# Performance work log

Hardware: AMD Instinct MI355X
Metric: run time of the kernel (lower is better)

The kernel has to match this reference:

```python
import jax, jax.numpy as jnp
import numpy as np

BLOCK = 32  # 2**basic_block

def _hadamard(n):
    H = np.array([[1.0]], dtype=np.float32)
    while H.shape[0] < n:
        H = np.block([[H, H], [H, -H]])
    return H


def setup_inputs() -> dict:
    key = jax.random.key(0)
    ks = jax.random.split(key, 9)
    B, T, I, Hd, O = 64, 512, 128, 1024, 128
    sgn = lambda k, shp: jnp.where(jax.random.normal(k, shp) >= 0, 1.0, -1.0).astype(jnp.float32)
    return {
        "x": jax.random.normal(ks[0], (B, T, I), dtype=jnp.float32),
        "W_in": jax.random.normal(ks[1], (I, Hd), dtype=jnp.float32) / np.sqrt(I),
        "s1": sgn(ks[2], (Hd,)),                      # Binadamard sign vector (layer 1)
        "b1": 0.01 * jax.random.normal(ks[3], (Hd,), dtype=jnp.float32),
        "s2": sgn(ks[4], (Hd,)),                      # Binadamard sign vector (layer 2, full)
        "b2": 0.01 * jax.random.normal(ks[5], (Hd,), dtype=jnp.float32),
        "Wbn": sgn(ks[6], (Hd, Hd)) / np.sqrt(Hd),    # BinaryNorm: sign(W)/sqrt(n), materialized
        "W_out": jax.random.normal(ks[7], (Hd, O), dtype=jnp.float32) / np.sqrt(Hd),
        "b_out": jax.random.normal(ks[8], (O,), dtype=jnp.float32),
    }


def reference(x, W_in, s1, b1, s2, b2, Wbn, W_out, b_out):
    B, T, _ = x.shape
    Hd = s1.shape[0]
    Hb = jnp.asarray(_hadamard(BLOCK) / np.sqrt(BLOCK), dtype=x.dtype)   # [32,32]
    Hf = jnp.asarray(_hadamard(Hd) / np.sqrt(Hd), dtype=x.dtype)         # [Hd,Hd]
    u = jnp.einsum('bti,ih->tbh', x, W_in)  # precompute input projections, time-major

    def step(carry, u_t):
        h1, h2 = carry
        # layer 1: block-diagonal sign*Hadamard recurrence + input
        h1 = s1 * (h1.reshape(B, -1, BLOCK) @ Hb).reshape(B, Hd) + b1 + u_t
        h1b = jax.nn.relu(h1)
        # layer 2: full sign*Hadamard recurrence + binary-norm projection of h1b
        h2 = s2 * (h2 @ Hf) + b2 + h1b @ Wbn
        return (h1, h2), None

    h0 = jnp.zeros((B, Hd), dtype=x.dtype)
    (_, h2), _ = jax.lax.scan(step, (h0, h0), u)
    h2b = jax.nn.relu(h2)
    return h2b @ W_out + b_out
```

## Files before the change

### kernel.cpp

```cpp
#include <hip/hip_runtime.h>

#define B_ 64
#define T_ 512
#define I_ 128
#define H_ 1024
#define O_ 128

typedef unsigned short u16;
typedef unsigned int u32;
typedef __attribute__((ext_vector_type(8))) short short8v;
typedef __attribute__((ext_vector_type(4))) float float4v;

typedef __attribute__((address_space(1))) const void gvoid_t;
typedef __attribute__((address_space(3))) void svoid_t;

__device__ __forceinline__ u16 f2bf(float f) {
  union { float f; u32 u; } v; v.f = f;
  u32 r = v.u + 0x7FFF + ((v.u >> 16) & 1);
  return (u16)(r >> 16);
}
__device__ __forceinline__ float bf2f(u16 b) {
  union { u32 u; float f; } v; v.u = ((u32)b) << 16;
  return v.f;
}
__device__ __forceinline__ float bits2f(u32 b) {
  union { u32 u; float f; } v; v.u = b;
  return v.f;
}

__device__ __forceinline__ float fwht32(float x, int lane) {
#pragma unroll
  for (int s = 1; s <= 16; s <<= 1) {
    const float y = __shfl_xor(x, s);
    x = (lane & s) ? (y - x) : (x + y);
  }
  return x;
}

__device__ __forceinline__ void fwht32_reg(float* x) {
#pragma unroll
  for (int s = 1; s < 32; s <<= 1)
#pragma unroll
    for (int i = 0; i < 32; ++i)
      if (!(i & s)) { const float a = x[i], b = x[i | s]; x[i] = a + b; x[i | s] = a - b; }
}

__device__ __forceinline__ void transpose32(float* x, float (*T)[33], int t) {
#pragma unroll
  for (int c = 0; c < 32; ++c) T[t][c] = x[c];
#pragma unroll
  for (int c = 0; c < 32; ++c) x[c] = T[c][t];
}

__global__ __launch_bounds__(256) void prep_all(const float* __restrict__ x, const float* __restrict__ Wbn,
                                                const float* __restrict__ W_in, u16* __restrict__ xT,
                                                u16* __restrict__ WbnT, u16* __restrict__ WinT) {
  __shared__ float tl[32][33];
  const int blk = blockIdx.x;
  const int tid = threadIdx.x;
  if (blk < 1024) {
    const int bx = blk & 31, by = blk >> 5;
    const int c = tid & 31, r8 = tid >> 5;
#pragma unroll
    for (int i = 0; i < 4; ++i) {
      const int r = r8 + i * 8;
      tl[r][c] = Wbn[(size_t)(by * 32 + r) * 1024 + bx * 32 + c];
    }
    __syncthreads();
#pragma unroll
    for (int i = 0; i < 4; ++i) {
      const int r = r8 + i * 8;
      WbnT[(size_t)(bx * 32 + r) * 1024 + by * 32 + c] = f2bf(tl[c][r]);
    }
  } else if (blk < 1152) {
    const int t2 = blk - 1024;
    const int bx = t2 & 31, by = t2 >> 5;
    const int c = tid & 31, r8 = tid >> 5;
#pragma unroll
    for (int i = 0; i < 4; ++i) {
      const int r = r8 + i * 8;
      tl[r][c] = W_in[(size_t)(by * 32 + r) * 1024 + bx * 32 + c];
    }
    __syncthreads();
#pragma unroll
    for (int i = 0; i < 4; ++i) {
      const int r = r8 + i * 8;
      WinT[(size_t)(bx * 32 + r) * 128 + by * 32 + c] = f2bf(tl[c][r]);
    }
  } else {
    const int idx = (blk - 1152) * 256 + tid;
    const int i = idx & (I_ - 1);
    const int r = idx >> 7;
    const int b = r & (B_ - 1);
    const int t = r >> 6;
    xT[idx] = f2bf(x[((size_t)b * T_ + t) * I_ + i]);
  }
}

template <int K, bool BIAS>
__global__ __launch_bounds__(512) void gemm_bf16(const u16* __restrict__ A, const u16* __restrict__ Bt,
                                                 u16* __restrict__ C, const float* __restrict__ bias) {
  __shared__ u16 As[128 * 64];
  __shared__ u16 Bs[256 * 64];
  const int tid = threadIdx.x;
  const int bm = blockIdx.x, bn = blockIdx.y;
  const int lane = tid & 63, w = tid >> 6;
  const int wr = w >> 2, wc = w & 3;
  const int l16 = lane & 15, lq = lane >> 4;

  float4v acc[4][4];
#pragma unroll
  for (int mi = 0; mi < 4; ++mi)
#pragma unroll
    for (int ni = 0; ni < 4; ++ni)
#pragma unroll
      for (int j = 0; j < 4; ++j) acc[mi][ni][j] = 0.f;

  const int lrow = lane >> 3;
  const int scol = (((lane & 7) ^ lrow) << 3);
  const u16* Ag = A + (size_t)(bm * 128 + w * 16 + lrow) * K + scol;
  const u16* Bg = Bt + (size_t)(bn * 256 + w * 32 + lrow) * K + scol;

  for (int k0 = 0; k0 < K; k0 += 64) {
    __syncthreads();
#pragma unroll
    for (int i = 0; i < 2; ++i)
      __builtin_amdgcn_global_load_lds((gvoid_t*)(Ag + k0 + (size_t)i * 8 * K),
                                       (svoid_t*)&As[(w * 16 + i * 8) * 64], 16, 0, 0);
#pragma unroll
    for (int i = 0; i < 4; ++i)
      __builtin_amdgcn_global_load_lds((gvoid_t*)(Bg + k0 + (size_t)i * 8 * K),
                                       (svoid_t*)&Bs[(w * 32 + i * 8) * 64], 16, 0, 0);
    __syncthreads();
#pragma unroll
    for (int ks = 0; ks < 2; ++ks) {
      short8v a[4], bf[4];
#pragma unroll
      for (int mi = 0; mi < 4; ++mi) {
        const int row = wr * 64 + mi * 16 + l16;
        a[mi] = *(const short8v*)&As[row * 64 + (((ks * 4 + lq) ^ (row & 7)) << 3)];
      }
#pragma unroll
      for (int ni = 0; ni < 4; ++ni) {
        const int row = wc * 64 + ni * 16 + l16;
        bf[ni] = *(const short8v*)&Bs[row * 64 + (((ks * 4 + lq) ^ (row & 7)) << 3)];
      }
#pragma unroll
      for (int mi = 0; mi < 4; ++mi)
#pragma unroll
        for (int ni = 0; ni < 4; ++ni)
          acc[mi][ni] = __builtin_amdgcn_mfma_f32_16x16x32_bf16(a[mi], bf[ni], acc[mi][ni], 0, 0, 0);
    }
  }

#pragma unroll
  for (int mi = 0; mi < 4; ++mi)
#pragma unroll
    for (int ni = 0; ni < 4; ++ni) {
      const int row = bm * 128 + wr * 64 + mi * 16 + lq * 4;
      const int col = bn * 256 + wc * 64 + ni * 16 + l16;
      const float bv = BIAS ? bias[col] : 0.f;
#pragma unroll
      for (int j = 0; j < 4; ++j) C[(size_t)(row + j) * H_ + col] = f2bf(acc[mi][ni][j] + bv);
    }
}

__global__ __launch_bounds__(1024) void h1_Pinit(const float* __restrict__ s1, float* __restrict__ P) {
  const int hb = blockIdx.x;
  const int tid = threadIdx.x;
  const int j = tid >> 5, r = tid & 31;
  const int lane = tid & 63;
  const float sc = s1[hb * 32 + r] * 0.17677669529663687f;
  float x = (r == j) ? 1.f : 0.f;
  for (int it = 0; it < 16; ++it) x = sc * fwht32(x, lane);
  P[(size_t)hb * 1024 + r * 32 + j] = x;
}

__global__ __launch_bounds__(64) void h1_local(const u16* __restrict__ u, const float* __restrict__ s1,
                                               float* __restrict__ Ybuf) {
  const int g = blockIdx.x * 64 + threadIdx.x;
  const int hb = g & 31, b = (g >> 5) & 63, chunk = g >> 11;
  float x[32], sc[32];
#pragma unroll
  for (int i = 0; i < 32; i += 4) {
    const float4 s4 = *(const float4*)&s1[hb * 32 + i];
    sc[i] = s4.x * 0.17677669529663687f;
    sc[i + 1] = s4.y * 0.17677669529663687f;
    sc[i + 2] = s4.z * 0.17677669529663687f;
    sc[i + 3] = s4.w * 0.17677669529663687f;
  }
#pragma unroll
  for (int i = 0; i < 32; ++i) x[i] = 0.f;
  const u16* up = u + ((size_t)(chunk * 16) * B_ + b) * H_ + hb * 32;
#pragma unroll 2
  for (int k = 0; k < 16; ++k) {
    u32 wv[16];
#pragma unroll
    for (int j = 0; j < 4; ++j) {
      const uint4 t4 = *(const uint4*)(up + (size_t)k * (B_ * H_) + j * 8);
      wv[4 * j] = t4.x; wv[4 * j + 1] = t4.y; wv[4 * j + 2] = t4.z; wv[4 * j + 3] = t4.w;
    }
    fwht32_reg(x);
#pragma unroll
    for (int i2 = 0; i2 < 16; ++i2) {
      x[2 * i2]     = fmaf(sc[2 * i2],     x[2 * i2],     bits2f(wv[i2] << 16));
      x[2 * i2 + 1] = fmaf(sc[2 * i2 + 1], x[2 * i2 + 1], bits2f(wv[i2] & 0xFFFF0000u));
    }
  }
  float* yp = Ybuf + (size_t)g * 32;
#pragma unroll
  for (int i = 0; i < 32; i += 4) {
    float4 o; o.x = x[i]; o.y = x[i + 1]; o.z = x[i + 2]; o.w = x[i + 3];
    *(float4*)(yp + i) = o;
  }
}

__global__ __launch_bounds__(64) void h1_carry(const float* __restrict__ P, const float* __restrict__ Ybuf,
                                               float* __restrict__ Zbuf) {
  const int hpair = blockIdx.x, b = blockIdx.y;
  const int lane = threadIdx.x;
  const int r = lane & 31, hb = hpair * 2 + (lane >> 5);
  const float* Prow = P + (size_t)hb * 1024 + r * 32;
  float pr[32];
#pragma unroll
  for (int j = 0; j < 32; ++j) pr[j] = Prow[j];
  float z = 0.f;
  const int base = lane & 32;
  for (int c = 0; c < 32; ++c) {
    Zbuf[(((size_t)c * 64 + b) * 32 + hb) * 32 + r] = z;
    if (c < 31) {
      const float yv = Ybuf[(((size_t)c * 64 + b) * 32 + hb) * 32 + r];
      float zn = 0.f;
#pragma unroll
      for (int j = 0; j < 32; ++j) zn = fmaf(pr[j], __shfl(z, base + j), zn);
      z = zn + yv;
    }
  }
}

__global__ __launch_bounds__(64) void h1_apply(u16* __restrict__ u, const float* __restrict__ s1,
                                               const float* __restrict__ Zbuf) {
  const int g = blockIdx.x * 64 + threadIdx.x;
  const int hb = g & 31, b = (g >> 5) & 63, chunk = g >> 11;
  float x[32], sc[32];
#pragma unroll
  for (int i = 0; i < 32; i += 4) {
    const float4 s4 = *(const float4*)&s1[hb * 32 + i];
    sc[i] = s4.x * 0.17677669529663687f;
    sc[i + 1] = s4.y * 0.17677669529663687f;
    sc[i + 2] = s4.z * 0.17677669529663687f;
    sc[i + 3] = s4.w * 0.17677669529663687f;
  }
  const float* zp = Zbuf + (size_t)g * 32;
#pragma unroll
  for (int i = 0; i < 32; i += 4) {
    const float4 z4 = *(const float4*)(zp + i);
    x[i] = z4.x; x[i + 1] = z4.y; x[i + 2] = z4.z; x[i + 3] = z4.w;
  }
  u16* up = u + ((size_t)(chunk * 16) * B_ + b) * H_ + hb * 32;
#pragma unroll 2
  for (int k = 0; k < 16; ++k) {
    u32 wv[16];
#pragma unroll
    for (int j = 0; j < 4; ++j) {
      const uint4 t4 = *(const uint4*)(up + (size_t)k * (B_ * H_) + j * 8);
      wv[4 * j] = t4.x; wv[4 * j + 1] = t4.y; wv[4 * j + 2] = t4.z; wv[4 * j + 3] = t4.w;
    }
    fwht32_reg(x);
#pragma unroll
    for (int i2 = 0; i2 < 16; ++i2) {
      x[2 * i2]     = fmaf(sc[2 * i2],     x[2 * i2],     bits2f(wv[i2] << 16));
      x[2 * i2 + 1] = fmaf(sc[2 * i2 + 1], x[2 * i2 + 1], bits2f(wv[i2] & 0xFFFF0000u));
    }
    u32 ov[16];
#pragma unroll
    for (int i2 = 0; i2 < 16; ++i2) {
      const u32 lo = f2bf(fmaxf(x[2 * i2], 0.f));
      const u32 hi = f2bf(fmaxf(x[2 * i2 + 1], 0.f));
      ov[i2] = lo | (hi << 16);
    }
#pragma unroll
    for (int j = 0; j < 4; ++j) {
      uint4 t4; t4.x = ov[4 * j]; t4.y = ov[4 * j + 1]; t4.z = ov[4 * j + 2]; t4.w = ov[4 * j + 3];
      *(uint4*)(up + (size_t)k * (B_ * H_) + j * 8) = t4;
    }
  }
}

__global__ __launch_bounds__(256) void fwht_chunk(const u16* __restrict__ V, const float* __restrict__ s2,
                                                  u16* __restrict__ A32, u16* __restrict__ Y) {
  __shared__ float tr[4][2][32][33];
  const int wv = threadIdx.x >> 6;
  const int lane = threadIdx.x & 63;
  const int slot = lane >> 5, t = lane & 31;
  float (*T)[33] = tr[wv][slot];
  const int gs = blockIdx.x * 8 + wv * 2 + slot;

  float x[32], s0[32], s1[32];
#pragma unroll
  for (int c = 0; c < 32; ++c) {
    s0[c] = s2[t * 32 + c] * 0.03125f;
    s1[c] = s2[c * 32 + t] * 0.03125f;
  }

  if (gs < 1024) {
    const int W = gs;
#pragma unroll
    for (int c = 0; c < 32; ++c) x[c] = (t * 32 + c == W) ? 1.f : 0.f;
    for (int j = 0; j < 32; ++j) {
      if (j & 1) {
#pragma unroll
        for (int c = 0; c < 32; ++c) x[c] *= s1[c];
      } else {
#pragma unroll
        for (int c = 0; c < 32; ++c) x[c] *= s0[c];
      }
      fwht32_reg(x);
      transpose32(x, T, t);
      fwht32_reg(x);
    }
    u16* dst = A32 + (size_t)W * H_ + t * 32;
    u32 ov[16];
#pragma unroll
    for (int c = 0; c < 16; ++c) ov[c] = (u32)f2bf(x[2 * c]) | ((u32)f2bf(x[2 * c + 1]) << 16);
#pragma unroll
    for (int j = 0; j < 4; ++j) {
      uint4 t4; t4.x = ov[4 * j]; t4.y = ov[4 * j + 1]; t4.z = ov[4 * j + 2]; t4.w = ov[4 * j + 3];
      *(uint4*)(dst + j * 8) = t4;
    }
  } else {
    const int s = gs - 1024;
    const int c0 = s >> 6, b = s & 63;
    const u16* Vbase = V + ((size_t)(c0 * 32) * B_ + b) * H_;
#pragma unroll
    for (int c = 0; c < 32; ++c) x[c] = 0.f;
    for (int j = 0; j < 32; ++j) {
      const u16* vrow = Vbase + (size_t)j * (B_ * H_);
      const int pe = (j + 1) & 1;
      u32 vpk[16];
      u16 vsc[32];
      if (pe == 0) {
#pragma unroll
        for (int q = 0; q < 4; ++q) {
          const uint4 t4 = *(const uint4*)(vrow + t * 32 + q * 8);
          vpk[4 * q] = t4.x; vpk[4 * q + 1] = t4.y; vpk[4 * q + 2] = t4.z; vpk[4 * q + 3] = t4.w;
        }
      } else {
#pragma unroll
        for (int c = 0; c < 32; ++c) vsc[c] = vrow[c * 32 + t];
      }
      fwht32_reg(x);
      transpose32(x, T, t);
      fwht32_reg(x);
      if (pe == 0) {
#pragma unroll
        for (int c = 0; c < 16; ++c) {
          x[2 * c]     = fmaf(s0[2 * c],     x[2 * c],     bits2f(vpk[c] << 16));
          x[2 * c + 1] = fmaf(s0[2 * c + 1], x[2 * c + 1], bits2f(vpk[c] & 0xFFFF0000u));
        }
      } else {
#pragma unroll
        for (int c = 0; c < 32; ++c) x[c] = fmaf(s1[c], x[c], bf2f(vsc[c]));
      }
    }
    u16* dst = Y + ((size_t)c0 * B_ + b) * H_ + t * 32;
    u32 ov[16];
#pragma unroll
    for (int c = 0; c < 16; ++c) ov[c] = (u32)f2bf(x[2 * c]) | ((u32)f2bf(x[2 * c + 1]) << 16);
#pragma unroll
    for (int j = 0; j < 4; ++j) {
      uint4 t4; t4.x = ov[4 * j]; t4.y = ov[4 * j + 1]; t4.z = ov[4 * j + 2]; t4.w = ov[4 * j + 3];
      *(uint4*)(dst + j * 8) = t4;
    }
  }
}

template <bool FIRST, bool LAST>
__global__ __launch_bounds__(256) void combine(const u16* __restrict__ Zold, const u16* __restrict__ Yc,
                                               const u16* __restrict__ A32, u16* __restrict__ Znew,
                                               float* __restrict__ h2out) {
  const int rt = blockIdx.x >> 6, nt = blockIdx.x & 63;
  const int tid = threadIdx.x;
  __shared__ float red[4][16][16];
  if (!FIRST) {
    const int w = tid >> 6, lane = tid & 63, l16 = lane & 15, lq = lane >> 4;
    float4v acc = {0.f, 0.f, 0.f, 0.f};
    const u16* Ap = Zold + (size_t)(rt * 16 + l16) * H_ + w * 256 + lq * 8;
    const u16* Bp = A32 + (size_t)(nt * 16 + l16) * H_ + w * 256 + lq * 8;
#pragma unroll
    for (int ks = 0; ks < 8; ++ks) {
      short8v a = *(const short8v*)(Ap + ks * 32);
      short8v bb = *(const short8v*)(Bp + ks * 32);
      acc = __builtin_amdgcn_mfma_f32_16x16x32_bf16(a, bb, acc, 0, 0, 0);
    }
#pragma unroll
    for (int j = 0; j < 4; ++j) red[w][lq * 4 + j][l16] = acc[j];
    __syncthreads();
  } else {
    __syncthreads();
  }
  const int row = tid >> 4, col = tid & 15;
  float s = 0.f;
  if (!FIRST) s = red[0][row][col] + red[1][row][col] + red[2][row][col] + red[3][row][col];
  const int b = rt * 16 + row, n = nt * 16 + col;
  s += bf2f(Yc[(size_t)b * H_ + n]);
  if (LAST) h2out[(size_t)b * H_ + n] = s;
  else Znew[(size_t)b * H_ + n] = f2bf(s);
}

__global__ __launch_bounds__(128) void final_out(const float* __restrict__ h2, const float* __restrict__ W_out,
                                                 const float* __restrict__ b_out, float* __restrict__ out) {
  __shared__ float hrow[H_];
  const int b = blockIdx.x, o = threadIdx.x;
  for (int i = o; i < H_; i += 128) hrow[i] = fmaxf(h2[(size_t)b * H_ + i], 0.f);
  __syncthreads();
  float acc = b_out[o];
  for (int h = 0; h < H_; ++h) acc = fmaf(hrow[h], W_out[(size_t)h * O_ + o], acc);
  out[b * O_ + o] = acc;
}

extern "C" void kernel_launch(void* const* d_in, const int* in_sizes, int n_in,
                              void* d_out, int out_size, void* d_ws, size_t ws_size,
                              hipStream_t stream) {
  const float* x     = (const float*)d_in[0];
  const float* W_in  = (const float*)d_in[1];
  const float* s1    = (const float*)d_in[2];
  const float* b1    = (const float*)d_in[3];
  const float* s2    = (const float*)d_in[4];
  const float* b2    = (const float*)d_in[5];
  const float* Wbn   = (const float*)d_in[6];
  const float* W_out = (const float*)d_in[7];
  const float* b_out = (const float*)d_in[8];
  float* out = (float*)d_out;

  char* ws = (char*)d_ws;
  u16* u      = (u16*)ws;
  u16* V      = (u16*)(ws + 67108864);
  float* P1   = (float*)(ws + 67108864);
  float* Zbuf = (float*)(ws + 69206016);
  u16* xT     = (u16*)(ws + 134217728);
  float* Ybuf = (float*)(ws + 134217728);
  u16* WbnT   = (u16*)(ws + 142606336);
  u16* WinT   = (u16*)(ws + 144703488);
  u16* A32    = (u16*)(ws + 134217728);
  u16* Y      = (u16*)(ws + 136314880);
  u16* Zb0    = (u16*)(ws + 138412032);
  u16* Zb1    = (u16*)(ws + 138543104);
  float* h2   = (float*)(ws + 138674176);

  prep_all<<<17536, 256, 0, stream>>>(x, Wbn, W_in, xT, WbnT, WinT);
  h1_Pinit<<<32, 1024, 0, stream>>>(s1, P1);
  gemm_bf16<128, true><<<dim3(256, 4), 512, 0, stream>>>(xT, WinT, u, b1);
  h1_local<<<1024, 64, 0, stream>>>(u, s1, Ybuf);
  h1_carry<<<dim3(16, 64), 64, 0, stream>>>(P1, Ybuf, Zbuf);
  h1_apply<<<1024, 64, 0, stream>>>(u, s1, Zbuf);
  gemm_bf16<1024, true><<<dim3(256, 4), 512, 0, stream>>>(u, WbnT, V, b2);
  fwht_chunk<<<256, 256, 0, stream>>>(V, s2, A32, Y);

  u16* Zb[2] = {Zb0, Zb1};
  combine<true, false><<<256, 256, 0, stream>>>(nullptr, Y, A32, Zb[0], nullptr);
  for (int c = 1; c < 15; ++c)
    combine<false, false><<<256, 256, 0, stream>>>(Zb[(c + 1) & 1], Y + (size_t)c * B_ * H_, A32,
                                                   Zb[c & 1], nullptr);
  combine<false, true><<<256, 256, 0, stream>>>(Zb[0], Y + (size_t)15 * B_ * H_, A32, nullptr, h2);

  final_out<<<64, 128, 0, stream>>>(h2, W_out, b_out, out);
}
```

Measured before the change: 309.5 us.

## Replace sequential chunk combine chain with log-depth tree using squared transition matrices

The 16 sequential combine launches become a binary-tree reduction. Each level pairs chunk states and multiplies by a doubled-power transition matrix (A32, A64, A128, A256), which is computed by repeated squaring with explicit transposes. This cuts the serial dependency chain from 16 launches to about 7, but adds three full 1024x1024 bf16 matrix squarings and extra rounding from squaring in bf16, which may hurt accuracy.

```diff
diff --git a/kernel.cpp b/kernel.cpp
--- a/kernel.cpp
+++ b/kernel.cpp
@@ -375,37 +375,93 @@
   }
 }
 
-template <bool FIRST, bool LAST>
-__global__ __launch_bounds__(256) void combine(const u16* __restrict__ Zold, const u16* __restrict__ Yc,
-                                               const u16* __restrict__ A32, u16* __restrict__ Znew,
-                                               float* __restrict__ h2out) {
+template <bool LAST>
+__device__ __forceinline__ void tree_tile(const u16* X, const u16* add, const u16* P,
+                                          u16* out, float* h2out, int rt, int nt, int tid,
+                                          float (*red)[16][16]) {
+  const int w = tid >> 6, lane = tid & 63, l16 = lane & 15, lq = lane >> 4;
+  float4v acc = {0.f, 0.f, 0.f, 0.f};
+  const u16* Ap = X + (size_t)(rt * 16 + l16) * H_ + w * 256 + lq * 8;
+  const u16* Bp = P + (size_t)(nt * 16 + l16) * H_ + w * 256 + lq * 8;
+#pragma unroll
+  for (int ks = 0; ks < 8; ++ks) {
+    short8v a = *(const short8v*)(Ap + ks * 32);
+    short8v bb = *(const short8v*)(Bp + ks * 32);
+    acc = __builtin_amdgcn_mfma_f32_16x16x32_bf16(a, bb, acc, 0, 0, 0);
+  }
+#pragma unroll
+  for (int j = 0; j < 4; ++j) red[w][lq * 4 + j][l16] = acc[j];
+  __syncthreads();
+  const int row = tid >> 4, col = tid & 15;
+  float s = red[0][row][col] + red[1][row][col] + red[2][row][col] + red[3][row][col];
+  s += bf2f(add[(size_t)(rt * 16 + row) * H_ + nt * 16 + col]);
+  if (LAST) h2out[(size_t)(rt * 16 + row) * H_ + nt * 16 + col] = s;
+  else out[(size_t)(rt * 16 + row) * H_ + nt * 16 + col] = f2bf(s);
+}
+
+__global__ __launch_bounds__(256) void t0_l1(const u16* __restrict__ A32, const u16* __restrict__ Y,
+                                             u16* __restrict__ A32T, u16* __restrict__ W1) {
+  const int tid = threadIdx.x;
+  if (blockIdx.x < 1024) {
+    __shared__ u16 tl[32][33];
+    const int bx = blockIdx.x & 31, by = blockIdx.x >> 5;
+    const int c = tid & 31, r8 = tid >> 5;
+#pragma unroll
+    for (int i = 0; i < 4; ++i) {
+      const int r = r8 + i * 8;
+      tl[r][c] = A32[(size_t)(by * 32 + r) * 1024 + bx * 32 + c];
+    }
+    __syncthreads();
+#pragma unroll
+    for (int i = 0; i < 4; ++i) {
+      const int r = r8 + i * 8;
+      A32T[(size_t)(bx * 32 + r) * 1024 + by * 32 + c] = tl[c][r];
+    }
+  } else {
+    __shared__ float red[4][16][16];
+    const int b2 = blockIdx.x - 1024;
+    const int j = b2 >> 8, tile = b2 & 255;
+    const int rt = tile >> 6, nt = tile & 63;
+    const size_t BH = (size_t)B_ * H_;
+    tree_tile<false>(Y + (size_t)(2 * j) * BH, Y + (size_t)(2 * j + 1) * BH, A32,
+                     W1 + (size_t)j * BH, nullptr, rt, nt, tid, red);
+  }
+}
+
+template <bool LAST>
+__global__ __launch_bounds__(256) void tree_level(const u16* __restrict__ Xin, const u16* __restrict__ P,
+                                                  u16* __restrict__ Xout, float* __restrict__ h2out) {
+  __shared__ float red[4][16][16];
+  const int j = blockIdx.y;
+  const int rt = blockIdx.x >> 6, nt = blockIdx.x & 63;
+  const size_t BH = (size_t)B_ * H_;
+  tree_tile<LAST>(Xin + (size_t)(2 * j) * BH, Xin + (size_t)(2 * j + 1) * BH, P,
+                  LAST ? nullptr : (Xout + (size_t)j * BH), h2out, rt, nt, threadIdx.x, red);
+}
+
+__global__ __launch_bounds__(256) void power_sq(const u16* __restrict__ X, const u16* __restrict__ XT,
+                                                u16* __restrict__ C, u16* __restrict__ CT) {
+  __shared__ float red[4][16][16];
   const int rt = blockIdx.x >> 6, nt = blockIdx.x & 63;
   const int tid = threadIdx.x;
-  __shared__ float red[4][16][16];
-  if (!FIRST) {
-    const int w = tid >> 6, lane = tid & 63, l16 = lane & 15, lq = lane >> 4;
-    float4v acc = {0.f, 0.f, 0.f, 0.f};
-    const u16* Ap = Zold + (size_t)(rt * 16 + l16) * H_ + w * 256 + lq * 8;
-    const u16* Bp = A32 + (size_t)(nt * 16 + l16) * H_ + w * 256 + lq * 8;
-#pragma unroll
-    for (int ks = 0; ks < 8; ++ks) {
-      short8v a = *(const short8v*)(Ap + ks * 32);
-      short8v bb = *(const short8v*)(Bp + ks * 32);
-      acc = __builtin_amdgcn_mfma_f32_16x16x32_bf16(a, bb, acc, 0, 0, 0);
-    }
-#pragma unroll
-    for (int j = 0; j < 4; ++j) red[w][lq * 4 + j][l16] = acc[j];
-    __syncthreads();
-  } else {
-    __syncthreads();
-  }
+  const int w = tid >> 6, lane = tid & 63, l16 = lane & 15, lq = lane >> 4;
+  float4v acc = {0.f, 0.f, 0.f, 0.f};
+  const u16* Ap = X + (size_t)(rt * 16 + l16) * 1024 + w * 256 + lq * 8;
+  const u16* Bp = XT + (size_t)(nt * 16 + l16) * 1024 + w * 256 + lq * 8;
+#pragma unroll
+  for (int ks = 0; ks < 8; ++ks) {
+    short8v a = *(const short8v*)(Ap + ks * 32);
+    short8v bb = *(const short8v*)(Bp + ks * 32);
+    acc = __builtin_amdgcn_mfma_f32_16x16x32_bf16(a, bb, acc, 0, 0, 0);
+  }
+#pragma unroll
+  for (int j = 0; j < 4; ++j) red[w][lq * 4 + j][l16] = acc[j];
+  __syncthreads();
   const int row = tid >> 4, col = tid & 15;
-  float s = 0.f;
-  if (!FIRST) s = red[0][row][col] + red[1][row][col] + red[2][row][col] + red[3][row][col];
-  const int b = rt * 16 + row, n = nt * 16 + col;
-  s += bf2f(Yc[(size_t)b * H_ + n]);
-  if (LAST) h2out[(size_t)b * H_ + n] = s;
-  else Znew[(size_t)b * H_ + n] = f2bf(s);
+  const float s = red[0][row][col] + red[1][row][col] + red[2][row][col] + red[3][row][col];
+  const u16 bv = f2bf(s);
+  C[(size_t)(rt * 16 + row) * 1024 + nt * 16 + col] = bv;
+  if (CT) CT[(size_t)(nt * 16 + col) * 1024 + rt * 16 + row] = bv;
 }
 
 __global__ __launch_bounds__(128) void final_out(const float* __restrict__ h2, const float* __restrict__ W_out,
@@ -438,15 +494,22 @@
   u16* V      = (u16*)(ws + 67108864);
   float* P1   = (float*)(ws + 67108864);
   float* Zbuf = (float*)(ws + 69206016);
+  u16* A64T   = (u16*)(ws + 67108864);
+  u16* A128   = (u16*)(ws + 69206016);
+  u16* A128T  = (u16*)(ws + 71303168);
+  u16* A256   = (u16*)(ws + 73400320);
+  u16* W1     = (u16*)(ws + 75497472);
+  u16* W2     = (u16*)(ws + 76546048);
+  u16* W3     = (u16*)(ws + 77070336);
   u16* xT     = (u16*)(ws + 134217728);
   float* Ybuf = (float*)(ws + 134217728);
+  u16* A32    = (u16*)(ws + 134217728);
+  u16* A32T   = (u16*)(ws + 136314880);
+  u16* A64    = (u16*)(ws + 138412032);
+  u16* Y      = (u16*)(ws + 140509184);
   u16* WbnT   = (u16*)(ws + 142606336);
   u16* WinT   = (u16*)(ws + 144703488);
-  u16* A32    = (u16*)(ws + 134217728);
-  u16* Y      = (u16*)(ws + 136314880);
-  u16* Zb0    = (u16*)(ws + 138412032);
-  u16* Zb1    = (u16*)(ws + 138543104);
-  float* h2   = (float*)(ws + 138674176);
+  float* h2   = (float*)(ws + 144965632);
 
   prep_all<<<17536, 256, 0, stream>>>(x, Wbn, W_in, xT, WbnT, WinT);
   h1_Pinit<<<32, 1024, 0, stream>>>(s1, P1);
@@ -457,12 +520,12 @@
   gemm_bf16<1024, true><<<dim3(256, 4), 512, 0, stream>>>(u, WbnT, V, b2);
   fwht_chunk<<<256, 256, 0, stream>>>(V, s2, A32, Y);
 
-  u16* Zb[2] = {Zb0, Zb1};
-  combine<true, false><<<256, 256, 0, stream>>>(nullptr, Y, A32, Zb[0], nullptr);
-  for (int c = 1; c < 15; ++c)
-    combine<false, false><<<256, 256, 0, stream>>>(Zb[(c + 1) & 1], Y + (size_t)c * B_ * H_, A32,
-                                                   Zb[c & 1], nullptr);
-  combine<false, true><<<256, 256, 0, stream>>>(Zb[0], Y + (size_t)15 * B_ * H_, A32, nullptr, h2);
-
+  t0_l1<<<3072, 256, 0, stream>>>(A32, Y, A32T, W1);
+  power_sq<<<4096, 256, 0, stream>>>(A32, A32T, A64, A64T);
+  tree_level<false><<<dim3(256, 4), 256, 0, stream>>>(W1, A64, W2, nullptr);
+  power_sq<<<4096, 256, 0, stream>>>(A64, A64T, A128, A128T);
+  tree_level<false><<<dim3(256, 2), 256, 0, stream>>>(W2, A128, W3, nullptr);
+  power_sq<<<4096, 256, 0, stream>>>(A128, A128T, A256, nullptr);
+  tree_level<true><<<dim3(256, 1), 256, 0, stream>>>(W3, A256, nullptr, h2);
   final_out<<<64, 128, 0, stream>>>(h2, W_out, b_out, out);
 }
```

Result: slower. 373.9 us (+20.8%).
